# Performance work log

Measured on AMD Instinct MI355X. Metric: run time of the kernel, lower is better.

## Reference

```python
import jax, jax.numpy as jnp
import numpy as np

# CrossAttention (DFFNet): 1x1 convs produce q,k from depth and v from rgb;
# full dense attention over hw spatial tokens: softmax(q^T k) then v @ mask^T.

def setup_inputs() -> dict:
    key = jax.random.key(0)
    ks = jax.random.split(key, 8)
    B, C, H, W = 4, 256, 64, 64
    Cqk = C // 8  # ratio=8 -> 32
    s = 0.02
    return {
        "rgb":   jax.random.normal(ks[0], (B, C, H, W), jnp.float32),
        "depth": jax.random.normal(ks[1], (B, C, H, W), jnp.float32),
        "Wq": jax.random.normal(ks[2], (Cqk, C), jnp.float32) * s,
        "bq": jax.random.normal(ks[3], (Cqk,), jnp.float32) * s,
        "Wk": jax.random.normal(ks[4], (Cqk, C), jnp.float32) * s,
        "bk": jax.random.normal(ks[5], (Cqk,), jnp.float32) * s,
        "Wv": jax.random.normal(ks[6], (C, C), jnp.float32) * s,
        "bv": jax.random.normal(ks[7], (C,), jnp.float32) * s,
    }


def reference(rgb, depth, Wq, bq, Wk, bk, Wv, bv):
    B, C, H, W = rgb.shape
    hw = H * W
    d = depth.reshape(B, C, hw)   # [B, C, hw]
    r = rgb.reshape(B, C, hw)     # [B, C, hw]
    # 1x1 convs == channel-mixing linear maps
    q = jnp.einsum('oc,bcn->bon', Wq, d) + bq[None, :, None]  # [B, Cqk, hw]
    k = jnp.einsum('oc,bcn->bon', Wk, d) + bk[None, :, None]  # [B, Cqk, hw]
    v = jnp.einsum('oc,bcn->bon', Wv, r) + bv[None, :, None]  # [B, C, hw]
    # scores: q^T k -> [B, hw, hw], softmax over last dim
    scores = jnp.einsum('bcn,bcm->bnm', q, k)
    mask = jax.nn.softmax(scores, axis=-1)
    # feat = v @ mask^T  -> [B, C, hw]
    feat = jnp.einsum('bcm,bnm->bcn', v, mask)
    return feat.reshape(B, C, H, W)
```

## Files before the change

kernel.cpp:

```cpp
#include <hip/hip_runtime.h>
#include <stdint.h>

#define L2E 1.44269504088896340736f

typedef _Float16 half8 __attribute__((ext_vector_type(8)));
typedef float floatx4 __attribute__((ext_vector_type(4)));
typedef float floatx16 __attribute__((ext_vector_type(16)));

static __device__ __forceinline__ unsigned short f32_to_f16u(float f) {
  union { _Float16 h; unsigned short s; } cv; cv.h = (_Float16)f; return cv.s;
}
static __device__ __forceinline__ _Float16 f32h(float f) { return (_Float16)f; }

__global__ __launch_bounds__(256, 5) void proj_kernel(
    const float* __restrict__ rgb,
    const float* __restrict__ depth,
    const float* __restrict__ Wq, const float* __restrict__ bq,
    const float* __restrict__ Wk, const float* __restrict__ bk,
    const float* __restrict__ Wv, const float* __restrict__ bv,
    unsigned short* __restrict__ qT,
    unsigned short* __restrict__ kT,
    unsigned short* __restrict__ v)
{
  __shared__ __align__(16) unsigned short sW[64 * 256];

  const int n0 = blockIdx.x * 64;
  const int b  = blockIdx.y;
  const int z  = blockIdx.z;
  const int t  = threadIdx.x;
  const int w  = t >> 6;
  const int lane = t & 63;
  const int l15 = lane & 15;
  const int q4  = lane >> 4;
  const int n_row = n0 + 16 * w + l15;

  const float* X = (z == 0) ? depth : rgb;
  const float* xb = X + (size_t)b * 256 * 4096;
  const float* xrow = xb + n_row;
  const int colbase = (z == 0) ? 0 : (z - 1) * 64;

#pragma unroll
  for (int it = 0; it < 8; it++) {
    int L = it * 256 + t;
    int og = L >> 5;
    int phys = L & 31;
    int ci = phys ^ (og & 7);
    const float* wr;
    if (z == 0) wr = (og < 32) ? (Wq + (size_t)og * 256) : (Wk + (size_t)(og - 32) * 256);
    else        wr = Wv + (size_t)(colbase + og) * 256;
    float4 w0 = *(const float4*)(wr + ci * 8);
    float4 w1 = *(const float4*)(wr + ci * 8 + 4);
    half8 h;
    h[0] = f32h(w0.x); h[1] = f32h(w0.y); h[2] = f32h(w0.z); h[3] = f32h(w0.w);
    h[4] = f32h(w1.x); h[5] = f32h(w1.y); h[6] = f32h(w1.z); h[7] = f32h(w1.w);
    *(half8*)&sW[(size_t)L * 8] = h;
  }

  float bias[4];
#pragma unroll
  for (int ct = 0; ct < 4; ct++) {
    int og = ct * 16 + l15;
    if (z == 0) bias[ct] = (og < 32) ? bq[og] : bk[og - 32];
    else        bias[ct] = bv[colbase + og];
  }
  __syncthreads();

  floatx4 acc[4];
#pragma unroll
  for (int i = 0; i < 4; i++) acc[i] = (floatx4){0.f, 0.f, 0.f, 0.f};

  float af[8];
#pragma unroll
  for (int j = 0; j < 8; j++) af[j] = xrow[(size_t)(q4 * 8 + j) * 4096];

#pragma unroll
  for (int ks = 0; ks < 8; ks++) {
    half8 a;
#pragma unroll
    for (int j = 0; j < 8; j++) a[j] = (_Float16)af[j];
    if (ks < 7) {
#pragma unroll
      for (int j = 0; j < 8; j++)
        af[j] = xrow[(size_t)(ks * 32 + 32 + q4 * 8 + j) * 4096];
    }
    const int ci = ks * 4 + q4;
#pragma unroll
    for (int ct = 0; ct < 4; ct++) {
      int og = ct * 16 + l15;
      half8 bf = *(const half8*)&sW[og * 256 + ((ci ^ (og & 7)) * 8)];
      acc[ct] = __builtin_amdgcn_mfma_f32_16x16x32_f16(a, bf, acc[ct], 0, 0, 0);
    }
  }

  __syncthreads();

  if (z == 0) {
#pragma unroll
    for (int ct = 0; ct < 4; ct++) {
      int og = ct * 16 + l15;
#pragma unroll
      for (int r = 0; r < 4; r++) {
        int n = n0 + 16 * w + q4 * 4 + r;
        unsigned short hv = f32_to_f16u(acc[ct][r] + bias[ct]);
        if (og < 32) qT[((size_t)b * 4096 + n) * 32 + og] = hv;
        else         kT[((size_t)b * 4096 + n) * 32 + (og - 32)] = hv;
      }
    }
  } else {
    unsigned short* tile = sW;
#pragma unroll
    for (int ct = 0; ct < 4; ct++) {
#pragma unroll
      for (int r = 0; r < 4; r++) {
        int co_l = ct * 16 + l15;
        int nl = 16 * w + q4 * 4 + r;
        tile[co_l * 72 + nl] = f32_to_f16u(acc[ct][r] + bias[ct]);
      }
    }
    __syncthreads();
#pragma unroll
    for (int it = 0; it < 2; it++) {
      int co_l = it * 32 + (t >> 3);
      int ch = t & 7;
      int4 val = *(const int4*)&tile[co_l * 72 + ch * 8];
      *(int4*)&v[((size_t)b * 256 + colbase + co_l) * 4096 + n0 + ch * 8] = val;
    }
  }
}

__global__ __launch_bounds__(256, 6) void attn_kernel(
    const unsigned short* __restrict__ qT,
    const unsigned short* __restrict__ kT,
    const unsigned short* __restrict__ v,
    unsigned short* __restrict__ Op,
    float* __restrict__ lW)
{
  __shared__ __align__(16) unsigned char smem[18432];
  unsigned short* sV = (unsigned short*)smem;
  unsigned short* sP = (unsigned short*)(smem + 8192);

  const int n0 = blockIdx.x * 64;
  const int b  = blockIdx.y;
  const int chunk = blockIdx.z >> 1;
  const int half  = blockIdx.z & 1;
  const int t  = threadIdx.x;
  const int w  = t >> 6;
  const int lane = t & 63;
  const int l15 = lane & 15;
  const int q4  = lane >> 4;
  const int l31 = lane & 31;
  const int hi  = lane >> 5;
  const int co0 = half * 128;

  const unsigned short* qrow = qT + ((size_t)b * 4096 + n0 + 16 * w + l15) * 32 + q4 * 8;
  half8 aq = *(const half8*)qrow;

  const unsigned short* vB = v  + (size_t)b * 256 * 4096 + (size_t)co0 * 4096;
  const unsigned short* kB = kT + (size_t)b * 4096 * 32;

  float lsum[4] = {0.f, 0.f, 0.f, 0.f};
  floatx16 acc[2];
#pragma unroll
  for (int nt = 0; nt < 2; nt++)
#pragma unroll
    for (int i = 0; i < 16; i++) acc[nt][i] = 0.f;
  const floatx4 zf = (floatx4){0.f, 0.f, 0.f, 0.f};

  const int mbase = chunk * 1024;
  for (int mi = 0; mi < 1024; mi += 32) {
    const int m0 = mbase + mi;
    half8 bk0 = *(const half8*)&kB[(size_t)(m0 + l15) * 32 + q4 * 8];
    half8 bk1 = *(const half8*)&kB[(size_t)(m0 + 16 + l15) * 32 + q4 * 8];

    __syncthreads();
#pragma unroll
    for (int j = 0; j < 2; j++) {
      int lin = j * 256 + t;
      int c = lin >> 2;
      int p = lin & 3;
      int lc = p ^ ((c >> 1) & 3);
      uint4 val = *(const uint4*)&vB[(size_t)c * 4096 + m0 + lc * 8];
      *(uint4*)&sV[lin * 8] = val;
    }
    __syncthreads();

    floatx4 s0 = __builtin_amdgcn_mfma_f32_16x16x32_f16(aq, bk0, zf, 0, 0, 0);
    floatx4 s1 = __builtin_amdgcn_mfma_f32_16x16x32_f16(aq, bk1, zf, 0, 0, 0);

    float p0[4], p1[4];
#pragma unroll
    for (int r = 0; r < 4; r++) {
      p0[r] = exp2f(s0[r] * L2E);
      p1[r] = exp2f(s1[r] * L2E);
      lsum[r] += p0[r] + p1[r];
    }
#pragma unroll
    for (int r = 0; r < 4; r++) {
      int row = w * 16 + q4 * 4 + r;
      sP[row * 40 + l15]      = f32_to_f16u(p0[r]);
      sP[row * 40 + 16 + l15] = f32_to_f16u(p1[r]);
    }
    __syncthreads();

    const int c_lw = w * 32 + l31;
#pragma unroll
    for (int kst = 0; kst < 2; kst++) {
      int lc = (kst * 2 + hi) ^ ((c_lw >> 1) & 3);
      half8 bvv = *(const half8*)&sV[(c_lw * 4 + lc) * 8];
#pragma unroll
      for (int nt = 0; nt < 2; nt++) {
        half8 ap = *(const half8*)&sP[(nt * 32 + l31) * 40 + kst * 16 + hi * 8];
        acc[nt] = __builtin_amdgcn_mfma_f32_32x32x16_f16(ap, bvv, acc[nt], 0, 0, 0);
      }
    }
  }

#pragma unroll
  for (int off = 1; off < 16; off <<= 1) {
#pragma unroll
    for (int r = 0; r < 4; r++) lsum[r] += __shfl_xor(lsum[r], off);
  }
  if (half == 0 && l15 == 0) {
#pragma unroll
    for (int r = 0; r < 4; r++)
      lW[((size_t)chunk * 4 + b) * 4096 + n0 + 16 * w + q4 * 4 + r] = lsum[r];
  }

  __syncthreads();
  unsigned short* sO = (unsigned short*)smem;
  const int co_l = w * 32 + l31;
#pragma unroll
  for (int nt = 0; nt < 2; nt++) {
#pragma unroll
    for (int g = 0; g < 4; g++) {
      int nl = nt * 32 + g * 8 + hi * 4;
      ushort4 pk;
      pk.x = f32_to_f16u(acc[nt][g * 4 + 0]);
      pk.y = f32_to_f16u(acc[nt][g * 4 + 1]);
      pk.z = f32_to_f16u(acc[nt][g * 4 + 2]);
      pk.w = f32_to_f16u(acc[nt][g * 4 + 3]);
      *(ushort4*)&sO[co_l * 72 + nl] = pk;
    }
  }
  __syncthreads();
#pragma unroll
  for (int s = 0; s < 4; s++) {
    int cl = s * 32 + (t >> 3);
    int ch = t & 7;
    int4 val = *(const int4*)&sO[cl * 72 + ch * 8];
    *(int4*)&Op[(((size_t)chunk * 4 + b) * 256 + co0 + cl) * 4096 + n0 + ch * 8] = val;
  }
}

__global__ __launch_bounds__(256) void combine_kernel(
    const unsigned short* __restrict__ Op,
    const float* __restrict__ lW,
    float* __restrict__ out)
{
  const int t = threadIdx.x;
  const int b = blockIdx.y;
  const int co = blockIdx.z;
  const size_t n8 = (size_t)blockIdx.x * 2048 + (size_t)t * 8;

  float sum[8] = {0.f, 0.f, 0.f, 0.f, 0.f, 0.f, 0.f, 0.f};
  float o[8]   = {0.f, 0.f, 0.f, 0.f, 0.f, 0.f, 0.f, 0.f};
#pragma unroll
  for (int ch = 0; ch < 4; ch++) {
    const float* lp = lW + ((size_t)ch * 4 + b) * 4096 + n8;
    float4 a0 = *(const float4*)lp;
    float4 a1 = *(const float4*)(lp + 4);
    sum[0] += a0.x; sum[1] += a0.y; sum[2] += a0.z; sum[3] += a0.w;
    sum[4] += a1.x; sum[5] += a1.y; sum[6] += a1.z; sum[7] += a1.w;
    half8 hv = *(const half8*)&Op[(((size_t)ch * 4 + b) * 256 + co) * 4096 + n8];
#pragma unroll
    for (int i = 0; i < 8; i++) o[i] += (float)hv[i];
  }
  float* op = out + ((size_t)b * 256 + co) * 4096 + n8;
  float4 r0, r1;
  r0.x = o[0] / sum[0]; r0.y = o[1] / sum[1]; r0.z = o[2] / sum[2]; r0.w = o[3] / sum[3];
  r1.x = o[4] / sum[4]; r1.y = o[5] / sum[5]; r1.z = o[6] / sum[6]; r1.w = o[7] / sum[7];
  *(float4*)op = r0;
  *(float4*)(op + 4) = r1;
}

extern "C" void kernel_launch(void* const* d_in, const int* in_sizes, int n_in,
                              void* d_out, int out_size, void* d_ws, size_t ws_size,
                              hipStream_t stream) {
  const float* rgb   = (const float*)d_in[0];
  const float* depth = (const float*)d_in[1];
  const float* Wq    = (const float*)d_in[2];
  const float* bq    = (const float*)d_in[3];
  const float* Wk    = (const float*)d_in[4];
  const float* bk    = (const float*)d_in[5];
  const float* Wv    = (const float*)d_in[6];
  const float* bv    = (const float*)d_in[7];
  float* out = (float*)d_out;

  unsigned short* qT = (unsigned short*)d_ws;
  unsigned short* kT = qT + (size_t)4 * 4096 * 32;
  unsigned short* vW = kT + (size_t)4 * 4096 * 32;
  unsigned short* Op = vW + (size_t)4 * 256 * 4096;
  float* lW = (float*)(Op + (size_t)4 * 4 * 256 * 4096);

  dim3 pg(64, 4, 5);
  proj_kernel<<<pg, 256, 0, stream>>>(rgb, depth, Wq, bq, Wk, bk, Wv, bv, qT, kT, vW);
  dim3 ag(64, 4, 8);
  attn_kernel<<<ag, 256, 0, stream>>>(qT, kT, vW, Op, lW);
  dim3 cg(2, 4, 256);
  combine_kernel<<<cg, 256, 0, stream>>>(Op, lW, out);
}
```

Measured before the change: 196.5 us.

## Register-prefetch V/K tiles, widen attention to all channels, stage proj input in LDS

The attention kernel now computes all 256 output channels per block instead of splitting channels across two blocks. This halves the recomputation of QK scores and exp and halves the grid. V and K tiles for the next step are prefetched into registers while the current step computes, and K is staged through swizzled LDS. The projection kernel now loads its input tile with coalesced float4 reads into padded LDS rather than strided per-row scalar loads. The cost is more LDS and more accumulator registers, with lowered launch bounds and occupancy.

Result: slower. 272.3 us (+38.6%).

```diff
diff --git a/kernel.cpp b/kernel.cpp
--- a/kernel.cpp
+++ b/kernel.cpp
@@ -12,7 +12,7 @@
 }
 static __device__ __forceinline__ _Float16 f32h(float f) { return (_Float16)f; }
 
-__global__ __launch_bounds__(256, 5) void proj_kernel(
+__global__ __launch_bounds__(256, 2) void proj_kernel(
     const float* __restrict__ rgb,
     const float* __restrict__ depth,
     const float* __restrict__ Wq, const float* __restrict__ bq,
@@ -23,6 +23,7 @@
     unsigned short* __restrict__ v)
 {
   __shared__ __align__(16) unsigned short sW[64 * 256];
+  __shared__ __align__(16) unsigned short sX[256 * 74];
 
   const int n0 = blockIdx.x * 64;
   const int b  = blockIdx.y;
@@ -32,11 +33,10 @@
   const int lane = t & 63;
   const int l15 = lane & 15;
   const int q4  = lane >> 4;
-  const int n_row = n0 + 16 * w + l15;
+  const int nl  = 16 * w + l15;
 
   const float* X = (z == 0) ? depth : rgb;
-  const float* xb = X + (size_t)b * 256 * 4096;
-  const float* xrow = xb + n_row;
+  const float* xb = X + (size_t)b * 256 * 4096 + n0;
   const int colbase = (z == 0) ? 0 : (z - 1) * 64;
 
 #pragma unroll
@@ -56,6 +56,17 @@
     *(half8*)&sW[(size_t)L * 8] = h;
   }
 
+#pragma unroll
+  for (int it = 0; it < 16; it++) {
+    int c = it * 16 + (t >> 4);
+    int nc = 4 * (t & 15);
+    float4 x4 = *(const float4*)&xb[(size_t)c * 4096 + nc];
+    ushort4 st;
+    st.x = f32_to_f16u(x4.x); st.y = f32_to_f16u(x4.y);
+    st.z = f32_to_f16u(x4.z); st.w = f32_to_f16u(x4.w);
+    *(ushort4*)&sX[c * 74 + nc] = st;
+  }
+
   float bias[4];
 #pragma unroll
   for (int ct = 0; ct < 4; ct++) {
@@ -69,20 +80,13 @@
 #pragma unroll
   for (int i = 0; i < 4; i++) acc[i] = (floatx4){0.f, 0.f, 0.f, 0.f};
 
-  float af[8];
-#pragma unroll
-  for (int j = 0; j < 8; j++) af[j] = xrow[(size_t)(q4 * 8 + j) * 4096];
-
+  const _Float16* sXh = (const _Float16*)sX;
 #pragma unroll
   for (int ks = 0; ks < 8; ks++) {
     half8 a;
 #pragma unroll
-    for (int j = 0; j < 8; j++) a[j] = (_Float16)af[j];
-    if (ks < 7) {
-#pragma unroll
-      for (int j = 0; j < 8; j++)
-        af[j] = xrow[(size_t)(ks * 32 + 32 + q4 * 8 + j) * 4096];
-    }
+    for (int j = 0; j < 8; j++)
+      a[j] = sXh[(ks * 32 + q4 * 8 + j) * 74 + nl];
     const int ci = ks * 4 + q4;
 #pragma unroll
     for (int ct = 0; ct < 4; ct++) {
@@ -113,8 +117,8 @@
 #pragma unroll
       for (int r = 0; r < 4; r++) {
         int co_l = ct * 16 + l15;
-        int nl = 16 * w + q4 * 4 + r;
-        tile[co_l * 72 + nl] = f32_to_f16u(acc[ct][r] + bias[ct]);
+        int nn = 16 * w + q4 * 4 + r;
+        tile[co_l * 72 + nn] = f32_to_f16u(acc[ct][r] + bias[ct]);
       }
     }
     __syncthreads();
@@ -128,21 +132,21 @@
   }
 }
 
-__global__ __launch_bounds__(256, 6) void attn_kernel(
+__global__ __launch_bounds__(256, 4) void attn_kernel(
     const unsigned short* __restrict__ qT,
     const unsigned short* __restrict__ kT,
     const unsigned short* __restrict__ v,
     unsigned short* __restrict__ Op,
     float* __restrict__ lW)
 {
-  __shared__ __align__(16) unsigned char smem[18432];
+  __shared__ __align__(16) unsigned char smem[36864];
   unsigned short* sV = (unsigned short*)smem;
-  unsigned short* sP = (unsigned short*)(smem + 8192);
+  unsigned short* sK = (unsigned short*)(smem + 16384);
+  unsigned short* sP = (unsigned short*)(smem + 18432);
 
   const int n0 = blockIdx.x * 64;
   const int b  = blockIdx.y;
-  const int chunk = blockIdx.z >> 1;
-  const int half  = blockIdx.z & 1;
+  const int chunk = blockIdx.z;
   const int t  = threadIdx.x;
   const int w  = t >> 6;
   const int lane = t & 63;
@@ -150,40 +154,69 @@
   const int q4  = lane >> 4;
   const int l31 = lane & 31;
   const int hi  = lane >> 5;
-  const int co0 = half * 128;
 
   const unsigned short* qrow = qT + ((size_t)b * 4096 + n0 + 16 * w + l15) * 32 + q4 * 8;
   half8 aq = *(const half8*)qrow;
 
-  const unsigned short* vB = v  + (size_t)b * 256 * 4096 + (size_t)co0 * 4096;
+  const unsigned short* vB = v  + (size_t)b * 256 * 4096;
   const unsigned short* kB = kT + (size_t)b * 4096 * 32;
 
   float lsum[4] = {0.f, 0.f, 0.f, 0.f};
-  floatx16 acc[2];
+  floatx16 acc[2][2];
 #pragma unroll
   for (int nt = 0; nt < 2; nt++)
 #pragma unroll
-    for (int i = 0; i < 16; i++) acc[nt][i] = 0.f;
+    for (int ct = 0; ct < 2; ct++)
+#pragma unroll
+      for (int i = 0; i < 16; i++) acc[nt][ct][i] = 0.f;
   const floatx4 zf = (floatx4){0.f, 0.f, 0.f, 0.f};
 
   const int mbase = chunk * 1024;
+
+  const int svc = (4 * 256 > 0) ? 0 : 0;
+  uint4 pv[4];
+  uint4 pk;
+#pragma unroll
+  for (int j = 0; j < 4; j++) {
+    int lin = j * 256 + t;
+    int c = lin >> 2;
+    int p = lin & 3;
+    int lc = p ^ ((c >> 1) & 3);
+    pv[j] = *(const uint4*)&vB[(size_t)c * 4096 + mbase + lc * 8];
+  }
+  if (t < 128) {
+    int m = t >> 2, p = t & 3, lc = p ^ ((m >> 1) & 3);
+    pk = *(const uint4*)&kB[(size_t)(mbase + m) * 32 + lc * 8];
+  }
+  (void)svc;
+
   for (int mi = 0; mi < 1024; mi += 32) {
-    const int m0 = mbase + mi;
-    half8 bk0 = *(const half8*)&kB[(size_t)(m0 + l15) * 32 + q4 * 8];
-    half8 bk1 = *(const half8*)&kB[(size_t)(m0 + 16 + l15) * 32 + q4 * 8];
-
     __syncthreads();
 #pragma unroll
-    for (int j = 0; j < 2; j++) {
-      int lin = j * 256 + t;
-      int c = lin >> 2;
-      int p = lin & 3;
-      int lc = p ^ ((c >> 1) & 3);
-      uint4 val = *(const uint4*)&vB[(size_t)c * 4096 + m0 + lc * 8];
-      *(uint4*)&sV[lin * 8] = val;
-    }
+    for (int j = 0; j < 4; j++)
+      *(uint4*)&sV[(j * 256 + t) * 8] = pv[j];
+    if (t < 128)
+      *(uint4*)&sK[t * 8] = pk;
     __syncthreads();
 
+    if (mi < 992) {
+      const int m0n = mbase + mi + 32;
+#pragma unroll
+      for (int j = 0; j < 4; j++) {
+        int lin = j * 256 + t;
+        int c = lin >> 2;
+        int p = lin & 3;
+        int lc = p ^ ((c >> 1) & 3);
+        pv[j] = *(const uint4*)&vB[(size_t)c * 4096 + m0n + lc * 8];
+      }
+      if (t < 128) {
+        int m = t >> 2, p = t & 3, lc = p ^ ((m >> 1) & 3);
+        pk = *(const uint4*)&kB[(size_t)(m0n + m) * 32 + lc * 8];
+      }
+    }
+
+    half8 bk0 = *(const half8*)&sK[l15 * 32 + ((q4 ^ ((l15 >> 1) & 3)) * 8)];
+    half8 bk1 = *(const half8*)&sK[(16 + l15) * 32 + ((q4 ^ (((16 + l15) >> 1) & 3)) * 8)];
     floatx4 s0 = __builtin_amdgcn_mfma_f32_16x16x32_f16(aq, bk0, zf, 0, 0, 0);
     floatx4 s1 = __builtin_amdgcn_mfma_f32_16x16x32_f16(aq, bk1, zf, 0, 0, 0);
 
@@ -197,20 +230,27 @@
 #pragma unroll
     for (int r = 0; r < 4; r++) {
       int row = w * 16 + q4 * 4 + r;
-      sP[row * 40 + l15]      = f32_to_f16u(p0[r]);
-      sP[row * 40 + 16 + l15] = f32_to_f16u(p1[r]);
+      sP[row * 42 + l15]      = f32_to_f16u(p0[r]);
+      sP[row * 42 + 16 + l15] = f32_to_f16u(p1[r]);
     }
     __syncthreads();
 
-    const int c_lw = w * 32 + l31;
 #pragma unroll
     for (int kst = 0; kst < 2; kst++) {
-      int lc = (kst * 2 + hi) ^ ((c_lw >> 1) & 3);
-      half8 bvv = *(const half8*)&sV[(c_lw * 4 + lc) * 8];
+      half8 bvv[2];
+#pragma unroll
+      for (int ct = 0; ct < 2; ct++) {
+        int co = w * 64 + ct * 32 + l31;
+        int lc = (kst * 2 + hi) ^ ((co >> 1) & 3);
+        bvv[ct] = *(const half8*)&sV[(co * 4 + lc) * 8];
+      }
 #pragma unroll
       for (int nt = 0; nt < 2; nt++) {
-        half8 ap = *(const half8*)&sP[(nt * 32 + l31) * 40 + kst * 16 + hi * 8];
-        acc[nt] = __builtin_amdgcn_mfma_f32_32x32x16_f16(ap, bvv, acc[nt], 0, 0, 0);
+        half8 ap = *(const half8*)&sP[(nt * 32 + l31) * 42 + kst * 16 + hi * 8];
+#pragma unroll
+        for (int ct = 0; ct < 2; ct++) {
+          acc[nt][ct] = __builtin_amdgcn_mfma_f32_32x32x16_f16(ap, bvv[ct], acc[nt][ct], 0, 0, 0);
+        }
       }
     }
   }
@@ -220,7 +260,7 @@
 #pragma unroll
     for (int r = 0; r < 4; r++) lsum[r] += __shfl_xor(lsum[r], off);
   }
-  if (half == 0 && l15 == 0) {
+  if (l15 == 0) {
 #pragma unroll
     for (int r = 0; r < 4; r++)
       lW[((size_t)chunk * 4 + b) * 4096 + n0 + 16 * w + q4 * 4 + r] = lsum[r];
@@ -228,27 +268,30 @@
 
   __syncthreads();
   unsigned short* sO = (unsigned short*)smem;
-  const int co_l = w * 32 + l31;
 #pragma unroll
   for (int nt = 0; nt < 2; nt++) {
 #pragma unroll
-    for (int g = 0; g < 4; g++) {
-      int nl = nt * 32 + g * 8 + hi * 4;
-      ushort4 pk;
-      pk.x = f32_to_f16u(acc[nt][g * 4 + 0]);
-      pk.y = f32_to_f16u(acc[nt][g * 4 + 1]);
-      pk.z = f32_to_f16u(acc[nt][g * 4 + 2]);
-      pk.w = f32_to_f16u(acc[nt][g * 4 + 3]);
-      *(ushort4*)&sO[co_l * 72 + nl] = pk;
+    for (int ct = 0; ct < 2; ct++) {
+      int co_l = w * 64 + ct * 32 + l31;
+#pragma unroll
+      for (int g = 0; g < 4; g++) {
+        int nn = nt * 32 + g * 8 + hi * 4;
+        ushort4 pkk;
+        pkk.x = f32_to_f16u(acc[nt][ct][g * 4 + 0]);
+        pkk.y = f32_to_f16u(acc[nt][ct][g * 4 + 1]);
+        pkk.z = f32_to_f16u(acc[nt][ct][g * 4 + 2]);
+        pkk.w = f32_to_f16u(acc[nt][ct][g * 4 + 3]);
+        *(ushort4*)&sO[co_l * 72 + nn] = pkk;
+      }
     }
   }
   __syncthreads();
 #pragma unroll
-  for (int s = 0; s < 4; s++) {
-    int cl = s * 32 + (t >> 3);
+  for (int s = 0; s < 8; s++) {
+    int co_l = s * 32 + (t >> 3);
     int ch = t & 7;
-    int4 val = *(const int4*)&sO[cl * 72 + ch * 8];
-    *(int4*)&Op[(((size_t)chunk * 4 + b) * 256 + co0 + cl) * 4096 + n0 + ch * 8] = val;
+    int4 val = *(const int4*)&sO[co_l * 72 + ch * 8];
+    *(int4*)&Op[(((size_t)chunk * 4 + b) * 256 + co_l) * 4096 + n0 + ch * 8] = val;
   }
 }
 
@@ -304,7 +347,7 @@
 
   dim3 pg(64, 4, 5);
   proj_kernel<<<pg, 256, 0, stream>>>(rgb, depth, Wq, bq, Wk, bk, Wv, bv, qT, kT, vW);
-  dim3 ag(64, 4, 8);
+  dim3 ag(64, 4, 4);
   attn_kernel<<<ag, 256, 0, stream>>>(qT, kT, vW, Op, lW);
   dim3 cg(2, 4, 256);
   combine_kernel<<<cg, 256, 0, stream>>>(Op, lW, out);
```
